# Optimization experiments

Hardware: AMD Instinct MI355X
Metric: run time of the kernel (lower is better)

The kernel has to match this reference:

```python
import jax, jax.numpy as jnp
import numpy as np

# --- static config (mirrors init_kwargs / letter_code) ---
BATCH, NODES, AMINO, ATOM = 64, 512, 64, 32
NTYPES = 20
# heavy-atom count minus 1 for the 20 standard amino acids (ARNDCQEGHILKMFPSTWYV)
RES_LENS = np.array([4, 10, 7, 7, 5, 8, 8, 3, 9, 7, 7, 8, 7, 10, 6, 5, 6, 13, 11, 6])
RMAX = int(RES_LENS.max())  # 13


def setup_inputs() -> dict:
    rng = np.random.default_rng(0)
    type_ids = rng.integers(0, NTYPES, size=NODES)           # metadata.seq as type indices
    lens = RES_LENS[type_ids]                                 # residue lengths per node
    valid = np.arange(RMAX)[None, :] < lens[:, None]          # (NODES, RMAX) valid-atom mask
    gather_idx = np.nonzero(valid.reshape(-1))[0]             # flat indices of real atoms

    key = jax.random.key(0)
    k1, k2 = jax.random.split(key)
    x = jax.random.normal(k1, (BATCH, NODES, AMINO, 3), dtype=jnp.float32)
    # stacked per-type TensLinear weights, zero-padded to RMAX residues of output
    W = jax.random.normal(k2, (NTYPES, AMINO, RMAX * ATOM), dtype=jnp.float32) * 0.05
    wmask = (np.arange(RMAX)[None, :, None] < RES_LENS[:, None, None])  # (NTYPES, RMAX, 1)
    wmask = np.broadcast_to(wmask, (NTYPES, RMAX, ATOM)).reshape(NTYPES, 1, RMAX * ATOM)
    W = W * jnp.asarray(wmask, dtype=jnp.float32)
    return {
        "x": x,
        "W": W,
        "type_ids": jnp.asarray(type_ids, dtype=jnp.int64),
        "gather_idx": jnp.asarray(gather_idx, dtype=jnp.int64),
    }


def reference(x, W, type_ids, gather_idx):
    # x: (B, N, amino, 3); W: (T, amino, RMAX*atom); equivariant linear on amino axis
    batch, nodes = x.shape[0], x.shape[1]
    Wg = W[type_ids]                                   # (N, amino, RMAX*atom) type dispatch
    out = jnp.einsum('bnav,naj->bnjv', x, Wg)          # (B, N, RMAX*atom, 3)
    out = out.reshape(batch, nodes * RMAX, ATOM, 3)    # padded per-residue atom blocks
    return out[:, gather_idx]                          # (B, total_atoms, atom, 3) = torch.cat
```

## Files before the change

### kernel.cpp

```cpp
#include <hip/hip_runtime.h>

typedef __bf16 bf16;
typedef __bf16 bf16x8 __attribute__((ext_vector_type(8)));
typedef float f32x4 __attribute__((ext_vector_type(4)));
typedef unsigned short u16;
typedef u16 u16x8 __attribute__((ext_vector_type(8)));
typedef unsigned int u32;

#define BATCH 64
#define NODES 512
#define AMINO 64
#define NTYPES 20
#define RMAX 13
#define NJT 26
#define PADA 72
#define CROWF 100

__constant__ int c_res_lens[NTYPES] = {4,10,7,7,5,8,8,3,9,7,7,8,7,10,6,5,6,13,11,6};

__device__ __forceinline__ u16 f2bf(float f) {
    u32 u; __builtin_memcpy(&u, &f, 4);
    u32 r = u + 0x7FFFu + ((u >> 16) & 1u);
    return (u16)(r >> 16);
}

__device__ __forceinline__ int detect_i64(const int* __restrict__ p) {
    int z = 0;
#pragma unroll
    for (int k = 0; k < 16; ++k) z |= p[2 * k + 1];
    return z == 0;
}
__device__ __forceinline__ int tid_at(const int* __restrict__ p, int n, int is64) {
    return p[is64 ? 2 * n : n];
}

__global__ __launch_bounds__(256) void prep_kernel(const float* __restrict__ W,
                                                   const int* __restrict__ type_ids,
                                                   u16* __restrict__ wswz,
                                                   int* __restrict__ S) {
    if (blockIdx.x < 260) {
        int g = blockIdx.x * 256 + threadIdx.x;
        if (g >= NTYPES * NJT * 2 * 64) return;
        int lane = g & 63;
        int chunk = g >> 6;
        int kh = chunk & 1;
        int tj = chunk >> 1;
        int t = tj / NJT;
        int jt = tj - t * NJT;
        int q = lane >> 4, c = lane & 15;
        int a0 = kh * 32 + q * 8;
        int j = jt * 16 + c;
        u16x8 v;
#pragma unroll
        for (int i = 0; i < 8; ++i)
            v[i] = f2bf(W[(size_t)(t * AMINO + a0 + i) * (RMAX * 32) + j]);
        *(u16x8*)(wswz + (size_t)chunk * 512 + lane * 8) = v;
    } else {
        __shared__ int s[256];
        int is64 = detect_i64(type_ids);
        int i = threadIdx.x;
        int la = c_res_lens[tid_at(type_ids, 2 * i, is64)];
        int lb = c_res_lens[tid_at(type_ids, 2 * i + 1, is64)];
        s[i] = la + lb;
        __syncthreads();
        for (int off = 1; off < 256; off <<= 1) {
            int v = (i >= off) ? s[i - off] : 0;
            __syncthreads();
            s[i] += v;
            __syncthreads();
        }
        int excl = s[i] - (la + lb);
        S[2 * i] = excl;
        S[2 * i + 1] = excl + la;
    }
}

__global__ __launch_bounds__(256) void main_kernel(const float* __restrict__ x,
                                                   const int* __restrict__ type_ids,
                                                   const int* __restrict__ S,
                                                   const u16* __restrict__ wswz,
                                                   float* __restrict__ out,
                                                   int G) {
    __shared__ __align__(16) u16 planes[3 * BATCH * PADA];
    __shared__ __align__(16) float cbuff[4][16 * CROWF];

    const int n = blockIdx.x;
    const int tid = threadIdx.x;
    const int is64 = detect_i64(type_ids);
    const int t = tid_at(type_ids, n, is64);
    const int len = c_res_lens[t];
    const int s0 = S[n];

#pragma unroll
    for (int it = 0; it < 12; ++it) {
        int E = (tid + it * 256) * 4;
        int b = E / 192;
        int rem = E - b * 192;
        f32x4 v4 = *(const f32x4*)(x + (size_t)(b * NODES + n) * 192 + rem);
#pragma unroll
        for (int i = 0; i < 4; ++i) {
            int e = rem + i;
            int a = e / 3;
            int vv = e - a * 3;
            planes[vv * (BATCH * PADA) + b * PADA + a] = f2bf(v4[i]);
        }
    }
    __syncthreads();

    const int w = tid >> 6;
    const int l = tid & 63;
    const int q = l >> 4;
    const int c = l & 15;

    union Frag { u16x8 u; bf16x8 b; };
    Frag Af[4][3][2];
#pragma unroll
    for (int m = 0; m < 4; ++m)
#pragma unroll
        for (int v = 0; v < 3; ++v)
#pragma unroll
            for (int kh = 0; kh < 2; ++kh)
                Af[m][v][kh].u = *(const u16x8*)(planes + v * (BATCH * PADA) +
                                                 (m * 16 + c) * PADA + kh * 32 + q * 8);

    float* cb = cbuff[w];

    for (int r = w; r < len; r += 4) {
        Frag Bf[2][2];
#pragma unroll
        for (int jj = 0; jj < 2; ++jj)
#pragma unroll
            for (int kh = 0; kh < 2; ++kh)
                Bf[jj][kh].u = *(const u16x8*)(wswz +
                                (size_t)((t * NJT + (2 * r + jj)) * 2 + kh) * 512 + l * 8);

        const int g = s0 + r;

#pragma unroll 1
        for (int m = 0; m < 4; ++m) {
            f32x4 acc[2][3];
            const f32x4 z = {0.f, 0.f, 0.f, 0.f};
#pragma unroll
            for (int jj = 0; jj < 2; ++jj)
#pragma unroll
                for (int v = 0; v < 3; ++v) {
                    f32x4 a0 = __builtin_amdgcn_mfma_f32_16x16x32_bf16(Af[m][v][0].b, Bf[jj][0].b, z, 0, 0, 0);
                    acc[jj][v] = __builtin_amdgcn_mfma_f32_16x16x32_bf16(Af[m][v][1].b, Bf[jj][1].b, a0, 0, 0, 0);
                }

#pragma unroll
            for (int jj = 0; jj < 2; ++jj)
#pragma unroll
                for (int v = 0; v < 3; ++v)
#pragma unroll
                    for (int reg = 0; reg < 4; ++reg)
                        cb[(q * 4 + reg) * CROWF + (jj * 16 + c) * 3 + v] =
                            acc[jj][v][reg];

            asm volatile("" ::: "memory");

#pragma unroll
            for (int it2 = 0; it2 < 6; ++it2) {
                int ck = it2 * 64 + l;
                int row = ck / 24;
                int c16 = ck - row * 24;
                uint4 d = *(const uint4*)((const char*)cb + row * (CROWF * 4) + c16 * 16);
                *(uint4*)((char*)out +
                          ((size_t)(m * 16 + row) * G + g) * 384 + c16 * 16) = d;
            }

            asm volatile("" ::: "memory");
        }
    }
}

extern "C" void kernel_launch(void* const* d_in, const int* in_sizes, int n_in,
                              void* d_out, int out_size, void* d_ws, size_t ws_size,
                              hipStream_t stream) {
    const float* x = (const float*)d_in[0];
    const float* W = (const float*)d_in[1];
    const int* type_ids = (const int*)d_in[2];
    int G = out_size / (BATCH * 32 * 3);

    int* S = (int*)d_ws;
    u16* wswz = (u16*)((char*)d_ws + 4096);

    prep_kernel<<<261, 256, 0, stream>>>(W, type_ids, wswz, S);
    main_kernel<<<NODES, 256, 0, stream>>>(x, type_ids, S, wswz, (float*)d_out, G);
}
```

Before: 152.9 us.

## Split each node across four blocks by batch chunk and store MFMA results directly

The main kernel now launches four blocks per node, each handling 16 of the 64 batch rows. This shrinks shared memory and raises parallelism and occupancy. The LDS staging buffer for output is removed, so each lane writes its accumulator values straight to global memory as scalar stores instead of coalesced 16-byte stores. The x load becomes scalar strided reads per lane. Weight fragments are now reloaded by four times as many blocks, and the output stores are less coalesced.

```diff
diff --git a/kernel.cpp b/kernel.cpp
--- a/kernel.cpp
+++ b/kernel.cpp
@@ -14,7 +14,6 @@
 #define RMAX 13
 #define NJT 26
 #define PADA 72
-#define CROWF 100
 
 __constant__ int c_res_lens[NTYPES] = {4,10,7,7,5,8,8,3,9,7,7,8,7,10,6,5,6,13,11,6};
 
@@ -81,49 +80,43 @@
                                                    const u16* __restrict__ wswz,
                                                    float* __restrict__ out,
                                                    int G) {
-    __shared__ __align__(16) u16 planes[3 * BATCH * PADA];
-    __shared__ __align__(16) float cbuff[4][16 * CROWF];
+    __shared__ __align__(16) u16 planes[3][16][PADA];
 
-    const int n = blockIdx.x;
+    const int bid = blockIdx.x;
+    const int n = bid >> 2;
+    const int m = bid & 3;
     const int tid = threadIdx.x;
+    const int w = tid >> 6;
+    const int l = tid & 63;
+
     const int is64 = detect_i64(type_ids);
     const int t = tid_at(type_ids, n, is64);
     const int len = c_res_lens[t];
     const int s0 = S[n];
 
 #pragma unroll
-    for (int it = 0; it < 12; ++it) {
-        int E = (tid + it * 256) * 4;
-        int b = E / 192;
-        int rem = E - b * 192;
-        f32x4 v4 = *(const f32x4*)(x + (size_t)(b * NODES + n) * 192 + rem);
-#pragma unroll
-        for (int i = 0; i < 4; ++i) {
-            int e = rem + i;
-            int a = e / 3;
-            int vv = e - a * 3;
-            planes[vv * (BATCH * PADA) + b * PADA + a] = f2bf(v4[i]);
-        }
+    for (int i = 0; i < 4; ++i) {
+        int b16 = i * 4 + w;
+        const float* src = x + ((size_t)(m * 16 + b16) * NODES + n) * 192 + l * 3;
+        float v0 = src[0];
+        float v1 = src[1];
+        float v2 = src[2];
+        planes[0][b16][l] = f2bf(v0);
+        planes[1][b16][l] = f2bf(v1);
+        planes[2][b16][l] = f2bf(v2);
     }
     __syncthreads();
 
-    const int w = tid >> 6;
-    const int l = tid & 63;
     const int q = l >> 4;
     const int c = l & 15;
 
     union Frag { u16x8 u; bf16x8 b; };
-    Frag Af[4][3][2];
+    Frag Af[3][2];
 #pragma unroll
-    for (int m = 0; m < 4; ++m)
+    for (int v = 0; v < 3; ++v)
 #pragma unroll
-        for (int v = 0; v < 3; ++v)
-#pragma unroll
-            for (int kh = 0; kh < 2; ++kh)
-                Af[m][v][kh].u = *(const u16x8*)(planes + v * (BATCH * PADA) +
-                                                 (m * 16 + c) * PADA + kh * 32 + q * 8);
-
-    float* cb = cbuff[w];
+        for (int kh = 0; kh < 2; ++kh)
+            Af[v][kh].u = *(const u16x8*)(&planes[v][c][kh * 32 + q * 8]);
 
     for (int r = w; r < len; r += 4) {
         Frag Bf[2][2];
@@ -136,40 +129,26 @@
 
         const int g = s0 + r;
 
-#pragma unroll 1
-        for (int m = 0; m < 4; ++m) {
-            f32x4 acc[2][3];
-            const f32x4 z = {0.f, 0.f, 0.f, 0.f};
+        f32x4 acc[2][3];
+        const f32x4 z = {0.f, 0.f, 0.f, 0.f};
 #pragma unroll
-            for (int jj = 0; jj < 2; ++jj)
+        for (int jj = 0; jj < 2; ++jj)
 #pragma unroll
-                for (int v = 0; v < 3; ++v) {
-                    f32x4 a0 = __builtin_amdgcn_mfma_f32_16x16x32_bf16(Af[m][v][0].b, Bf[jj][0].b, z, 0, 0, 0);
-                    acc[jj][v] = __builtin_amdgcn_mfma_f32_16x16x32_bf16(Af[m][v][1].b, Bf[jj][1].b, a0, 0, 0, 0);
-                }
+            for (int v = 0; v < 3; ++v) {
+                f32x4 a0 = __builtin_amdgcn_mfma_f32_16x16x32_bf16(Af[v][0].b, Bf[jj][0].b, z, 0, 0, 0);
+                acc[jj][v] = __builtin_amdgcn_mfma_f32_16x16x32_bf16(Af[v][1].b, Bf[jj][1].b, a0, 0, 0, 0);
+            }
 
 #pragma unroll
-            for (int jj = 0; jj < 2; ++jj)
+        for (int reg = 0; reg < 4; ++reg) {
+            float* rowp = out + ((size_t)(m * 16 + q * 4 + reg) * G + g) * 96;
 #pragma unroll
-                for (int v = 0; v < 3; ++v)
-#pragma unroll
-                    for (int reg = 0; reg < 4; ++reg)
-                        cb[(q * 4 + reg) * CROWF + (jj * 16 + c) * 3 + v] =
-                            acc[jj][v][reg];
-
-            asm volatile("" ::: "memory");
-
-#pragma unroll
-            for (int it2 = 0; it2 < 6; ++it2) {
-                int ck = it2 * 64 + l;
-                int row = ck / 24;
-                int c16 = ck - row * 24;
-                uint4 d = *(const uint4*)((const char*)cb + row * (CROWF * 4) + c16 * 16);
-                *(uint4*)((char*)out +
-                          ((size_t)(m * 16 + row) * G + g) * 384 + c16 * 16) = d;
+            for (int jj = 0; jj < 2; ++jj) {
+                float* p = rowp + (jj * 16 + c) * 3;
+                p[0] = acc[jj][0][reg];
+                p[1] = acc[jj][1][reg];
+                p[2] = acc[jj][2][reg];
             }
-
-            asm volatile("" ::: "memory");
         }
     }
 }
@@ -186,5 +165,5 @@
     u16* wswz = (u16*)((char*)d_ws + 4096);
 
     prep_kernel<<<261, 256, 0, stream>>>(W, type_ids, wswz, S);
-    main_kernel<<<NODES, 256, 0, stream>>>(x, type_ids, S, wswz, (float*)d_out, G);
+    main_kernel<<<NODES * 4, 256, 0, stream>>>(x, type_ids, S, wswz, (float*)d_out, G);
 }
```

Result: faster. 127.6 us (-16.5%).
